# Performance work log

Measured on AMD Instinct MI355X. Metric: run time of the kernel, lower is better.

Reference implementation:

```python
import jax, jax.numpy as jnp
import numpy as np

EPS = 1e-6

def _rmsnorm(h, w):
    # RMSNorm: h * rsqrt(mean(h^2)) * w
    var = jnp.mean(jnp.square(h), axis=-1, keepdims=True)
    return h * jax.lax.rsqrt(var + EPS) * w

def setup_inputs() -> dict:
    key = jax.random.key(0)
    ks = jax.random.split(key, 9)
    B, N, L, D, C = 2, 4096, 256, 2048, 6
    s = 0.02
    return {
        "x": jax.random.normal(ks[0], (B, N, D), jnp.float32),
        "text_emb": jax.random.normal(ks[1], (B, L, D), jnp.float32),
        "Wc": jax.random.normal(ks[2], (C, D), jnp.float32) * s,
        "Wq": jax.random.normal(ks[3], (D, D), jnp.float32) * s,
        "Wk": jax.random.normal(ks[4], (D, D), jnp.float32) * s,
        "Wv": jax.random.normal(ks[5], (D, D), jnp.float32) * s,
        "Wo": jax.random.normal(ks[6], (D, D), jnp.float32) * s,
        "blend_weights": jnp.ones((C,), jnp.float32) / C + jax.random.normal(ks[7], (C,), jnp.float32) * 0.1,
        "surreal_gate": jnp.zeros((1,), jnp.float32),
        "norm_weight": jnp.ones((D,), jnp.float32),
        "is_surreal": 1,
    }

def reference(x, text_emb, Wc, Wq, Wk, Wv, Wo, blend_weights, surreal_gate, norm_weight, is_surreal):
    B, N, D = x.shape
    # soft concept clustering over text tokens
    cluster_logits = jnp.einsum('bld,cd->blc', text_emb, Wc)
    cluster_weights = jax.nn.softmax(cluster_logits, axis=-1)
    concept_reps = jnp.einsum('blc,bld->bcd', cluster_weights, text_emb)  # (B,C,D)
    # SDPA with a single key/value per concept: softmax over 1 key == 1, so the
    # attention output is exactly v broadcast over the N query tokens (q and k
    # cancel out of the math entirely; their grads are zero).
    v = jnp.einsum('bcd,ed->bce', concept_reps, Wv)  # (B,C,D) == per-concept output
    blend = jax.nn.softmax(blend_weights, axis=0)
    fused_bd = jnp.einsum('c,bcd->bd', blend, v)  # (B,D)
    if is_surreal:
        gate = jax.nn.sigmoid(surreal_gate)  # (1,)
        contradiction = jnp.var(v, axis=1, ddof=1)  # torch .var() is unbiased
        fused_bd = fused_bd + gate * contradiction * 0.3
    # broadcast to (B,N,D) as the torch module materializes, then norm + out_proj
    fused = jnp.broadcast_to(fused_bd[:, None, :], (B, N, D))
    out = jnp.einsum('bnd,ed->bne', _rmsnorm(fused, norm_weight), Wo)
    return x + out
```

## Files before the change

kernel.cpp:

```cpp
#include <hip/hip_runtime.h>
#include <hip/hip_bf16.h>

#define BB 2
#define NN 4096
#define LL 256
#define DD 2048
#define CC 6
#define EPSF 1e-6f

__device__ __forceinline__ float dot4(float4 a, float4 b) {
    return a.x * b.x + a.y * b.y + a.z * b.z + a.w * b.w;
}

__device__ __forceinline__ void keep4(float4 v) {
    asm volatile("" :: "v"(v.x), "v"(v.y), "v"(v.z), "v"(v.w));
}

__global__ __launch_bounds__(256) void k_cluster(const float* __restrict__ te,
                                                 const float* __restrict__ Wc,
                                                 float* __restrict__ cw,
                                                 const float4* __restrict__ x4) {
    const int tid = threadIdx.x;
    if (blockIdx.x >= 512) {
        size_t i = (size_t)(blockIdx.x - 512) * 256 + tid;
#pragma unroll
        for (int k = 0; k < 16; ++k, i += 512 * 256) keep4(x4[i]);
        return;
    }
    const int row = blockIdx.x;
    const float4* t4 = (const float4*)(te + (size_t)row * DD);
    float p[CC];
#pragma unroll
    for (int c = 0; c < CC; ++c) p[c] = 0.f;
#pragma unroll
    for (int it = 0; it < 2; ++it) {
        const int i = it * 256 + tid;
        const float4 xv = t4[i];
#pragma unroll
        for (int c = 0; c < CC; ++c)
            p[c] += dot4(xv, ((const float4*)(Wc + (size_t)c * DD))[i]);
    }
#pragma unroll
    for (int c = 0; c < CC; ++c)
        for (int off = 32; off; off >>= 1) p[c] += __shfl_down(p[c], off);
    __shared__ float sred[4][CC];
    const int lane = tid & 63, wid = tid >> 6;
    if (lane == 0) {
#pragma unroll
        for (int c = 0; c < CC; ++c) sred[wid][c] = p[c];
    }
    __syncthreads();
    if (tid == 0) {
        float lg[CC], m = -1e30f;
#pragma unroll
        for (int c = 0; c < CC; ++c) {
            lg[c] = sred[0][c] + sred[1][c] + sred[2][c] + sred[3][c];
            m = fmaxf(m, lg[c]);
        }
        float s = 0.f;
#pragma unroll
        for (int c = 0; c < CC; ++c) { lg[c] = __expf(lg[c] - m); s += lg[c]; }
        const float inv = 1.f / s;
#pragma unroll
        for (int c = 0; c < CC; ++c) cw[row * CC + c] = lg[c] * inv;
    }
}

__global__ __launch_bounds__(256) void k_creps(const float* __restrict__ te,
                                               const float* __restrict__ cw,
                                               float* __restrict__ cr,
                                               const float4* __restrict__ x4) {
    const int tid = threadIdx.x;
    if (blockIdx.x >= 64) {
        const size_t HALF4 = (size_t)BB * NN * DD / 8;
        size_t i = HALF4 + (size_t)(blockIdx.x - 64) * 256 + tid;
#pragma unroll
        for (int k = 0; k < 16; ++k, i += 512 * 256) keep4(x4[i]);
        return;
    }
    const int b = blockIdx.x >> 5;
    const int d0 = (blockIdx.x & 31) * 64;
    const int lane = tid & 63, wid = tid >> 6;
    __shared__ float scw[LL * CC];
    __shared__ float sacc[4][64][CC];
    for (int i = tid; i < LL * CC; i += 256) scw[i] = cw[b * LL * CC + i];
    __syncthreads();
    float acc[CC];
#pragma unroll
    for (int c = 0; c < CC; ++c) acc[c] = 0.f;
    const float* tb = te + ((size_t)b * LL + wid * 64) * DD + d0 + lane;
    for (int l = 0; l < 64; ++l) {
        const float xv = tb[(size_t)l * DD];
        const int gl = wid * 64 + l;
#pragma unroll
        for (int c = 0; c < CC; ++c) acc[c] = fmaf(scw[gl * CC + c], xv, acc[c]);
    }
#pragma unroll
    for (int c = 0; c < CC; ++c) sacc[wid][lane][c] = acc[c];
    __syncthreads();
    if (tid < 64) {
#pragma unroll
        for (int c = 0; c < CC; ++c) {
            const float s = sacc[0][tid][c] + sacc[1][tid][c] +
                            sacc[2][tid][c] + sacc[3][tid][c];
            cr[((size_t)b * CC + c) * DD + d0 + tid] = s;
        }
    }
}

__global__ __launch_bounds__(256) void k_vfuse(const float* __restrict__ cr,
                                               const float* __restrict__ Wv,
                                               const float* __restrict__ blendw,
                                               const float* __restrict__ sgate,
                                               const int* __restrict__ issur,
                                               float* __restrict__ fused,
                                               const float4* __restrict__ Wo4) {
    const int tid = threadIdx.x;
    if (blockIdx.x >= 256) {
        size_t i = (size_t)(blockIdx.x - 256) * 256 + tid;
#pragma unroll
        for (int k = 0; k < 16; ++k, i += 256 * 256) keep4(Wo4[i]);
        return;
    }
    const int lane = tid & 63, wid = tid >> 6;
    const int e0 = blockIdx.x * 8 + wid * 2;
    float acc[BB][2][CC];
#pragma unroll
    for (int b = 0; b < BB; ++b)
#pragma unroll
        for (int j = 0; j < 2; ++j)
#pragma unroll
            for (int c = 0; c < CC; ++c) acc[b][j][c] = 0.f;
#pragma unroll
    for (int it = 0; it < 8; ++it) {
        const int d = it * 256 + lane * 4;
        const float4 w0 = *(const float4*)(Wv + (size_t)e0 * DD + d);
        const float4 w1 = *(const float4*)(Wv + (size_t)(e0 + 1) * DD + d);
#pragma unroll
        for (int b = 0; b < BB; ++b)
#pragma unroll
            for (int c = 0; c < CC; ++c) {
                const float4 cv = *(const float4*)(cr + ((size_t)b * CC + c) * DD + d);
                acc[b][0][c] += dot4(cv, w0);
                acc[b][1][c] += dot4(cv, w1);
            }
    }
#pragma unroll
    for (int b = 0; b < BB; ++b)
#pragma unroll
        for (int j = 0; j < 2; ++j)
#pragma unroll
            for (int c = 0; c < CC; ++c)
                for (int off = 32; off; off >>= 1)
                    acc[b][j][c] += __shfl_down(acc[b][j][c], off);
    if (lane == 0) {
        float bw[CC], m = -1e30f;
#pragma unroll
        for (int c = 0; c < CC; ++c) { bw[c] = blendw[c]; m = fmaxf(m, bw[c]); }
        float s = 0.f;
#pragma unroll
        for (int c = 0; c < CC; ++c) { bw[c] = __expf(bw[c] - m); s += bw[c]; }
        const float inv = 1.f / s;
#pragma unroll
        for (int c = 0; c < CC; ++c) bw[c] *= inv;
        const float gate = 1.f / (1.f + __expf(-sgate[0]));
        const int sur = issur[0];
#pragma unroll
        for (int b = 0; b < BB; ++b)
#pragma unroll
            for (int j = 0; j < 2; ++j) {
                float f = 0.f, mean = 0.f;
#pragma unroll
                for (int c = 0; c < CC; ++c) {
                    f = fmaf(bw[c], acc[b][j][c], f);
                    mean += acc[b][j][c];
                }
                mean *= (1.f / CC);
                float var = 0.f;
#pragma unroll
                for (int c = 0; c < CC; ++c) {
                    const float dv = acc[b][j][c] - mean;
                    var = fmaf(dv, dv, var);
                }
                var *= (1.f / (CC - 1));
                if (sur) f = fmaf(gate * var, 0.3f, f);
                fused[b * DD + e0 + j] = f;
            }
    }
}

__global__ __launch_bounds__(256) void k_rmsout(const float* __restrict__ fused,
                                                const float* __restrict__ nw,
                                                const float* __restrict__ Wo,
                                                float* __restrict__ o) {
    const int tid = threadIdx.x;
    const int lane = tid & 63, wid = tid >> 6;
    float ss[BB];
#pragma unroll
    for (int b = 0; b < BB; ++b) ss[b] = 0.f;
#pragma unroll
    for (int k = 0; k < DD / 256; ++k) {
        const int d = k * 256 + tid;
#pragma unroll
        for (int b = 0; b < BB; ++b) {
            const float v = fused[b * DD + d];
            ss[b] = fmaf(v, v, ss[b]);
        }
    }
#pragma unroll
    for (int b = 0; b < BB; ++b)
        for (int off = 32; off; off >>= 1) ss[b] += __shfl_down(ss[b], off);
    __shared__ float sred[4][BB];
    __shared__ float sscale[BB];
    if (lane == 0) {
#pragma unroll
        for (int b = 0; b < BB; ++b) sred[wid][b] = ss[b];
    }
    __syncthreads();
    if (tid == 0) {
#pragma unroll
        for (int b = 0; b < BB; ++b) {
            const float tot = sred[0][b] + sred[1][b] + sred[2][b] + sred[3][b];
            sscale[b] = rsqrtf(tot * (1.f / DD) + EPSF);
        }
    }
    __syncthreads();
    const int e = blockIdx.x * 4 + wid;
    float acc[BB];
#pragma unroll
    for (int b = 0; b < BB; ++b) acc[b] = 0.f;
#pragma unroll
    for (int it = 0; it < DD / 256; ++it) {
        const int d = it * 256 + lane * 4;
        const float4 wv = *(const float4*)(Wo + (size_t)e * DD + d);
        const float4 nv = *(const float4*)(nw + d);
        float4 t;
        t.x = wv.x * nv.x; t.y = wv.y * nv.y; t.z = wv.z * nv.z; t.w = wv.w * nv.w;
#pragma unroll
        for (int b = 0; b < BB; ++b) {
            const float4 fv = *(const float4*)(fused + (size_t)b * DD + d);
            acc[b] += dot4(fv, t);
        }
    }
#pragma unroll
    for (int b = 0; b < BB; ++b) {
        for (int off = 32; off; off >>= 1) acc[b] += __shfl_down(acc[b], off);
        if (lane == 0) o[b * DD + e] = acc[b] * sscale[b];
    }
}

__global__ __launch_bounds__(256) void k_add(const float* __restrict__ x,
                                             const float* __restrict__ o,
                                             float* __restrict__ out) {
    const float4* x4 = (const float4*)x;
    const float4* o4 = (const float4*)o;
    float4* out4 = (float4*)out;
    size_t f = (size_t)blockIdx.x * 256 + threadIdx.x;
#pragma unroll
    for (int k = 0; k < 8; ++k, f += (size_t)2048 * 256) {
        const int e4 = (int)(f & (DD / 4 - 1));
        const int b = (int)(f >> 21);
        const float4 xv = x4[f];
        const float4 ov = o4[b * (DD / 4) + e4];
        float4 r;
        r.x = xv.x + ov.x; r.y = xv.y + ov.y;
        r.z = xv.z + ov.z; r.w = xv.w + ov.w;
        out4[f] = r;
    }
}

extern "C" void kernel_launch(void* const* d_in, const int* in_sizes, int n_in,
                              void* d_out, int out_size, void* d_ws, size_t ws_size,
                              hipStream_t stream) {
    const float* x  = (const float*)d_in[0];
    const float* te = (const float*)d_in[1];
    const float* Wc = (const float*)d_in[2];
    const float* Wv = (const float*)d_in[5];
    const float* Wo = (const float*)d_in[6];
    const float* bw = (const float*)d_in[7];
    const float* sg = (const float*)d_in[8];
    const float* nw = (const float*)d_in[9];
    const int* isur = (const int*)d_in[10];
    float* out = (float*)d_out;

    float* ws     = (float*)d_ws;
    float* cw     = ws;
    float* cr     = ws + 4096;
    float* fusedv = ws + 4096 + 24576;
    float* o      = fusedv + 4096;

    hipLaunchKernelGGL(k_cluster, dim3(1024), dim3(256), 0, stream,
                       te, Wc, cw, (const float4*)x);
    hipLaunchKernelGGL(k_creps,   dim3(576),  dim3(256), 0, stream,
                       te, cw, cr, (const float4*)x);
    hipLaunchKernelGGL(k_vfuse,   dim3(512),  dim3(256), 0, stream,
                       cr, Wv, bw, sg, isur, fusedv, (const float4*)Wo);
    hipLaunchKernelGGL(k_rmsout,  dim3(DD / 4), dim3(256), 0, stream,
                       fusedv, nw, Wo, o);
    hipLaunchKernelGGL(k_add,     dim3(2048), dim3(256), 0, stream, x, o, out);
}
```

Baseline: 58.06 us.

## Drop cache-prefetch blocks, widen per-wave rows in GEMV kernels, nontemporal add

Removes the extra blocks in the first three kernels that prefetched x and Wo into cache while the small kernels ran. Each wave in the Wv and Wo GEMV kernels now computes four output rows instead of two or one, using fewer blocks and reusing the loaded activation vectors. The final broadcast add uses nontemporal loads and stores. Without the prefetch, x must stream from HBM during the add, and the GEMVs run with lower occupancy across fewer blocks.

```diff
diff --git a/kernel.cpp b/kernel.cpp
--- a/kernel.cpp
+++ b/kernel.cpp
@@ -8,25 +8,16 @@
 #define CC 6
 #define EPSF 1e-6f
 
+typedef float floatx4 __attribute__((ext_vector_type(4)));
+
 __device__ __forceinline__ float dot4(float4 a, float4 b) {
     return a.x * b.x + a.y * b.y + a.z * b.z + a.w * b.w;
 }
 
-__device__ __forceinline__ void keep4(float4 v) {
-    asm volatile("" :: "v"(v.x), "v"(v.y), "v"(v.z), "v"(v.w));
-}
-
 __global__ __launch_bounds__(256) void k_cluster(const float* __restrict__ te,
                                                  const float* __restrict__ Wc,
-                                                 float* __restrict__ cw,
-                                                 const float4* __restrict__ x4) {
-    const int tid = threadIdx.x;
-    if (blockIdx.x >= 512) {
-        size_t i = (size_t)(blockIdx.x - 512) * 256 + tid;
-#pragma unroll
-        for (int k = 0; k < 16; ++k, i += 512 * 256) keep4(x4[i]);
-        return;
-    }
+                                                 float* __restrict__ cw) {
+    const int tid = threadIdx.x;
     const int row = blockIdx.x;
     const float4* t4 = (const float4*)(te + (size_t)row * DD);
     float p[CC];
@@ -68,16 +59,8 @@
 
 __global__ __launch_bounds__(256) void k_creps(const float* __restrict__ te,
                                                const float* __restrict__ cw,
-                                               float* __restrict__ cr,
-                                               const float4* __restrict__ x4) {
-    const int tid = threadIdx.x;
-    if (blockIdx.x >= 64) {
-        const size_t HALF4 = (size_t)BB * NN * DD / 8;
-        size_t i = HALF4 + (size_t)(blockIdx.x - 64) * 256 + tid;
-#pragma unroll
-        for (int k = 0; k < 16; ++k, i += 512 * 256) keep4(x4[i]);
-        return;
-    }
+                                               float* __restrict__ cr) {
+    const int tid = threadIdx.x;
     const int b = blockIdx.x >> 5;
     const int d0 = (blockIdx.x & 31) * 64;
     const int lane = tid & 63, wid = tid >> 6;
@@ -113,42 +96,37 @@
                                                const float* __restrict__ blendw,
                                                const float* __restrict__ sgate,
                                                const int* __restrict__ issur,
-                                               float* __restrict__ fused,
-                                               const float4* __restrict__ Wo4) {
-    const int tid = threadIdx.x;
-    if (blockIdx.x >= 256) {
-        size_t i = (size_t)(blockIdx.x - 256) * 256 + tid;
-#pragma unroll
-        for (int k = 0; k < 16; ++k, i += 256 * 256) keep4(Wo4[i]);
-        return;
-    }
-    const int lane = tid & 63, wid = tid >> 6;
-    const int e0 = blockIdx.x * 8 + wid * 2;
-    float acc[BB][2][CC];
-#pragma unroll
-    for (int b = 0; b < BB; ++b)
-#pragma unroll
-        for (int j = 0; j < 2; ++j)
+                                               float* __restrict__ fused) {
+    const int tid = threadIdx.x;
+    const int lane = tid & 63, wid = tid >> 6;
+    const int e0 = (blockIdx.x * 4 + wid) * 4;
+    float acc[BB][4][CC];
+#pragma unroll
+    for (int b = 0; b < BB; ++b)
+#pragma unroll
+        for (int j = 0; j < 4; ++j)
 #pragma unroll
             for (int c = 0; c < CC; ++c) acc[b][j][c] = 0.f;
 #pragma unroll
     for (int it = 0; it < 8; ++it) {
         const int d = it * 256 + lane * 4;
-        const float4 w0 = *(const float4*)(Wv + (size_t)e0 * DD + d);
-        const float4 w1 = *(const float4*)(Wv + (size_t)(e0 + 1) * DD + d);
+        float4 w[4];
+#pragma unroll
+        for (int j = 0; j < 4; ++j)
+            w[j] = *(const float4*)(Wv + (size_t)(e0 + j) * DD + d);
 #pragma unroll
         for (int b = 0; b < BB; ++b)
 #pragma unroll
             for (int c = 0; c < CC; ++c) {
                 const float4 cv = *(const float4*)(cr + ((size_t)b * CC + c) * DD + d);
-                acc[b][0][c] += dot4(cv, w0);
-                acc[b][1][c] += dot4(cv, w1);
+#pragma unroll
+                for (int j = 0; j < 4; ++j) acc[b][j][c] += dot4(cv, w[j]);
             }
     }
 #pragma unroll
     for (int b = 0; b < BB; ++b)
 #pragma unroll
-        for (int j = 0; j < 2; ++j)
+        for (int j = 0; j < 4; ++j)
 #pragma unroll
             for (int c = 0; c < CC; ++c)
                 for (int off = 32; off; off >>= 1)
@@ -168,7 +146,7 @@
 #pragma unroll
         for (int b = 0; b < BB; ++b)
 #pragma unroll
-            for (int j = 0; j < 2; ++j) {
+            for (int j = 0; j < 4; ++j) {
                 float f = 0.f, mean = 0.f;
 #pragma unroll
                 for (int c = 0; c < CC; ++c) {
@@ -225,47 +203,55 @@
         }
     }
     __syncthreads();
-    const int e = blockIdx.x * 4 + wid;
-    float acc[BB];
-#pragma unroll
-    for (int b = 0; b < BB; ++b) acc[b] = 0.f;
-#pragma unroll
-    for (int it = 0; it < DD / 256; ++it) {
+    const int e0 = (blockIdx.x * 4 + wid) * 4;
+    float acc[BB][4];
+#pragma unroll
+    for (int b = 0; b < BB; ++b)
+#pragma unroll
+        for (int j = 0; j < 4; ++j) acc[b][j] = 0.f;
+#pragma unroll
+    for (int it = 0; it < 8; ++it) {
         const int d = it * 256 + lane * 4;
-        const float4 wv = *(const float4*)(Wo + (size_t)e * DD + d);
         const float4 nv = *(const float4*)(nw + d);
-        float4 t;
-        t.x = wv.x * nv.x; t.y = wv.y * nv.y; t.z = wv.z * nv.z; t.w = wv.w * nv.w;
+        float4 w[4];
+#pragma unroll
+        for (int j = 0; j < 4; ++j) {
+            const float4 wv = *(const float4*)(Wo + (size_t)(e0 + j) * DD + d);
+            w[j].x = wv.x * nv.x; w[j].y = wv.y * nv.y;
+            w[j].z = wv.z * nv.z; w[j].w = wv.w * nv.w;
+        }
 #pragma unroll
         for (int b = 0; b < BB; ++b) {
             const float4 fv = *(const float4*)(fused + (size_t)b * DD + d);
-            acc[b] += dot4(fv, t);
-        }
-    }
-#pragma unroll
-    for (int b = 0; b < BB; ++b) {
-        for (int off = 32; off; off >>= 1) acc[b] += __shfl_down(acc[b], off);
-        if (lane == 0) o[b * DD + e] = acc[b] * sscale[b];
-    }
+#pragma unroll
+            for (int j = 0; j < 4; ++j) acc[b][j] += dot4(fv, w[j]);
+        }
+    }
+#pragma unroll
+    for (int b = 0; b < BB; ++b)
+#pragma unroll
+        for (int j = 0; j < 4; ++j) {
+            float v = acc[b][j];
+            for (int off = 32; off; off >>= 1) v += __shfl_down(v, off);
+            if (lane == 0) o[b * DD + e0 + j] = v * sscale[b];
+        }
 }
 
 __global__ __launch_bounds__(256) void k_add(const float* __restrict__ x,
                                              const float* __restrict__ o,
                                              float* __restrict__ out) {
-    const float4* x4 = (const float4*)x;
-    const float4* o4 = (const float4*)o;
-    float4* out4 = (float4*)out;
+    const floatx4* x4 = (const floatx4*)x;
+    const floatx4* o4 = (const floatx4*)o;
+    floatx4* out4 = (floatx4*)out;
     size_t f = (size_t)blockIdx.x * 256 + threadIdx.x;
 #pragma unroll
     for (int k = 0; k < 8; ++k, f += (size_t)2048 * 256) {
         const int e4 = (int)(f & (DD / 4 - 1));
         const int b = (int)(f >> 21);
-        const float4 xv = x4[f];
-        const float4 ov = o4[b * (DD / 4) + e4];
-        float4 r;
-        r.x = xv.x + ov.x; r.y = xv.y + ov.y;
-        r.z = xv.z + ov.z; r.w = xv.w + ov.w;
-        out4[f] = r;
+        const floatx4 xv = __builtin_nontemporal_load(&x4[f]);
+        const floatx4 ov = o4[b * (DD / 4) + e4];
+        const floatx4 r = xv + ov;
+        __builtin_nontemporal_store(r, &out4[f]);
     }
 }
 
@@ -289,13 +275,11 @@
     float* fusedv = ws + 4096 + 24576;
     float* o      = fusedv + 4096;
 
-    hipLaunchKernelGGL(k_cluster, dim3(1024), dim3(256), 0, stream,
-                       te, Wc, cw, (const float4*)x);
-    hipLaunchKernelGGL(k_creps,   dim3(576),  dim3(256), 0, stream,
-                       te, cw, cr, (const float4*)x);
-    hipLaunchKernelGGL(k_vfuse,   dim3(512),  dim3(256), 0, stream,
-                       cr, Wv, bw, sg, isur, fusedv, (const float4*)Wo);
-    hipLaunchKernelGGL(k_rmsout,  dim3(DD / 4), dim3(256), 0, stream,
+    hipLaunchKernelGGL(k_cluster, dim3(BB * LL), dim3(256), 0, stream, te, Wc, cw);
+    hipLaunchKernelGGL(k_creps,   dim3(BB * 32), dim3(256), 0, stream, te, cw, cr);
+    hipLaunchKernelGGL(k_vfuse,   dim3(128), dim3(256), 0, stream,
+                       cr, Wv, bw, sg, isur, fusedv);
+    hipLaunchKernelGGL(k_rmsout,  dim3(128), dim3(256), 0, stream,
                        fusedv, nw, Wo, o);
     hipLaunchKernelGGL(k_add,     dim3(2048), dim3(256), 0, stream, x, o, out);
 }
```

Measured after the change: 73.68 us. 1.27x slower.

## Fuse front-end stages into one cooperative kernel with grid syncs

Applied to the files above, without the earlier changes.

Replaces the four small pre-processing kernels (cluster softmax, concept reps, V projection/fuse, RMSNorm+out proj) with one cooperative persistent kernel that separates the stages with grid-wide syncs, keeping the old kernels as a fallback. It also drops the L2 prefetch side-blocks (keep4 loads of x and Wo) that were piggybacked on the earlier kernels. The aim is to cut launch gaps between the dependent small stages. In exchange the grid-sync overhead is added, and the lost prefetch of x may make the final add kernel more DRAM-bound.

```diff
diff --git a/kernel.cpp b/kernel.cpp
--- a/kernel.cpp
+++ b/kernel.cpp
@@ -1,5 +1,8 @@
 #include <hip/hip_runtime.h>
 #include <hip/hip_bf16.h>
+#include <hip/hip_cooperative_groups.h>
+
+namespace cg = cooperative_groups;
 
 #define BB 2
 #define NN 4096
@@ -12,21 +15,217 @@
     return a.x * b.x + a.y * b.y + a.z * b.z + a.w * b.w;
 }
 
-__device__ __forceinline__ void keep4(float4 v) {
-    asm volatile("" :: "v"(v.x), "v"(v.y), "v"(v.z), "v"(v.w));
+__global__ __launch_bounds__(256) void k_front(
+    const float* __restrict__ te, const float* __restrict__ Wc,
+    const float* __restrict__ Wv, const float* __restrict__ Wo,
+    const float* __restrict__ blendw, const float* __restrict__ sgate,
+    const int* __restrict__ issur, const float* __restrict__ nw,
+    float* __restrict__ cw, float* __restrict__ cr,
+    float* __restrict__ fused, float* __restrict__ o)
+{
+    cg::grid_group gg = cg::this_grid();
+    __shared__ float smem[3072];
+    const int G = gridDim.x;
+    const int tid = threadIdx.x;
+    const int lane = tid & 63, wid = tid >> 6;
+
+    for (int row = blockIdx.x; row < BB * LL; row += G) {
+        const float4* t4 = (const float4*)(te + (size_t)row * DD);
+        float p[CC];
+#pragma unroll
+        for (int c = 0; c < CC; ++c) p[c] = 0.f;
+#pragma unroll
+        for (int it = 0; it < 2; ++it) {
+            const int i = it * 256 + tid;
+            const float4 xv = t4[i];
+#pragma unroll
+            for (int c = 0; c < CC; ++c)
+                p[c] += dot4(xv, ((const float4*)(Wc + (size_t)c * DD))[i]);
+        }
+#pragma unroll
+        for (int c = 0; c < CC; ++c)
+            for (int off = 32; off; off >>= 1) p[c] += __shfl_down(p[c], off);
+        if (lane == 0) {
+#pragma unroll
+            for (int c = 0; c < CC; ++c) smem[wid * CC + c] = p[c];
+        }
+        __syncthreads();
+        if (tid == 0) {
+            float lg[CC], m = -1e30f;
+#pragma unroll
+            for (int c = 0; c < CC; ++c) {
+                lg[c] = smem[c] + smem[CC + c] + smem[2 * CC + c] + smem[3 * CC + c];
+                m = fmaxf(m, lg[c]);
+            }
+            float s = 0.f;
+#pragma unroll
+            for (int c = 0; c < CC; ++c) { lg[c] = __expf(lg[c] - m); s += lg[c]; }
+            const float inv = 1.f / s;
+#pragma unroll
+            for (int c = 0; c < CC; ++c) cw[row * CC + c] = lg[c] * inv;
+        }
+        __syncthreads();
+    }
+    gg.sync();
+
+    for (int u = blockIdx.x; u < 64; u += G) {
+        const int b = u >> 5;
+        const int d0 = (u & 31) * 64;
+        float* scw = smem;
+        float* sacc = smem + 1536;
+        for (int i = tid; i < LL * CC; i += 256) scw[i] = cw[b * LL * CC + i];
+        __syncthreads();
+        float acc[CC];
+#pragma unroll
+        for (int c = 0; c < CC; ++c) acc[c] = 0.f;
+        const float* tb = te + ((size_t)b * LL + wid * 64) * DD + d0 + lane;
+        for (int l = 0; l < 64; ++l) {
+            const float xv = tb[(size_t)l * DD];
+            const int gl = wid * 64 + l;
+#pragma unroll
+            for (int c = 0; c < CC; ++c) acc[c] = fmaf(scw[gl * CC + c], xv, acc[c]);
+        }
+#pragma unroll
+        for (int c = 0; c < CC; ++c) sacc[(wid * 64 + lane) * CC + c] = acc[c];
+        __syncthreads();
+        if (tid < 64) {
+#pragma unroll
+            for (int c = 0; c < CC; ++c) {
+                const float s = sacc[(0 * 64 + tid) * CC + c] + sacc[(1 * 64 + tid) * CC + c] +
+                                sacc[(2 * 64 + tid) * CC + c] + sacc[(3 * 64 + tid) * CC + c];
+                cr[((size_t)b * CC + c) * DD + d0 + tid] = s;
+            }
+        }
+        __syncthreads();
+    }
+    gg.sync();
+
+    for (int u = blockIdx.x; u < 512; u += G) {
+        const int e = u * 4 + wid;
+        float acc[BB][CC];
+#pragma unroll
+        for (int b = 0; b < BB; ++b)
+#pragma unroll
+            for (int c = 0; c < CC; ++c) acc[b][c] = 0.f;
+#pragma unroll
+        for (int it = 0; it < 8; ++it) {
+            const int d = it * 256 + lane * 4;
+            const float4 wv = *(const float4*)(Wv + (size_t)e * DD + d);
+#pragma unroll
+            for (int b = 0; b < BB; ++b)
+#pragma unroll
+                for (int c = 0; c < CC; ++c) {
+                    const float4 cv = *(const float4*)(cr + ((size_t)b * CC + c) * DD + d);
+                    acc[b][c] += dot4(cv, wv);
+                }
+        }
+#pragma unroll
+        for (int b = 0; b < BB; ++b)
+#pragma unroll
+            for (int c = 0; c < CC; ++c)
+                for (int off = 32; off; off >>= 1)
+                    acc[b][c] += __shfl_down(acc[b][c], off);
+        if (lane == 0) {
+            float bw[CC], m = -1e30f;
+#pragma unroll
+            for (int c = 0; c < CC; ++c) { bw[c] = blendw[c]; m = fmaxf(m, bw[c]); }
+            float s = 0.f;
+#pragma unroll
+            for (int c = 0; c < CC; ++c) { bw[c] = __expf(bw[c] - m); s += bw[c]; }
+            const float inv = 1.f / s;
+#pragma unroll
+            for (int c = 0; c < CC; ++c) bw[c] *= inv;
+            const float gate = 1.f / (1.f + __expf(-sgate[0]));
+            const int sur = issur[0];
+#pragma unroll
+            for (int b = 0; b < BB; ++b) {
+                float f = 0.f, mean = 0.f;
+#pragma unroll
+                for (int c = 0; c < CC; ++c) {
+                    f = fmaf(bw[c], acc[b][c], f);
+                    mean += acc[b][c];
+                }
+                mean *= (1.f / CC);
+                float var = 0.f;
+#pragma unroll
+                for (int c = 0; c < CC; ++c) {
+                    const float dv = acc[b][c] - mean;
+                    var = fmaf(dv, dv, var);
+                }
+                var *= (1.f / (CC - 1));
+                if (sur) f = fmaf(gate * var, 0.3f, f);
+                fused[b * DD + e] = f;
+            }
+        }
+    }
+    gg.sync();
+
+    {
+        float ss[BB];
+#pragma unroll
+        for (int b = 0; b < BB; ++b) ss[b] = 0.f;
+#pragma unroll
+        for (int k = 0; k < DD / 256; ++k) {
+            const int d = k * 256 + tid;
+#pragma unroll
+            for (int b = 0; b < BB; ++b) {
+                const float v = fused[b * DD + d];
+                ss[b] = fmaf(v, v, ss[b]);
+            }
+        }
+#pragma unroll
+        for (int b = 0; b < BB; ++b)
+            for (int off = 32; off; off >>= 1) ss[b] += __shfl_down(ss[b], off);
+        if (lane == 0) {
+#pragma unroll
+            for (int b = 0; b < BB; ++b) smem[wid * BB + b] = ss[b];
+        }
+        __syncthreads();
+        if (tid == 0) {
+#pragma unroll
+            for (int b = 0; b < BB; ++b) {
+                const float tot = smem[0 * BB + b] + smem[1 * BB + b] +
+                                  smem[2 * BB + b] + smem[3 * BB + b];
+                smem[8 + b] = rsqrtf(tot * (1.f / DD) + EPSF);
+            }
+        }
+        __syncthreads();
+        const float scl0 = smem[8], scl1 = smem[9];
+        for (int u = blockIdx.x; u < 512; u += G) {
+            const int e = u * 4 + wid;
+            float acc[BB];
+#pragma unroll
+            for (int b = 0; b < BB; ++b) acc[b] = 0.f;
+#pragma unroll
+            for (int it = 0; it < 8; ++it) {
+                const int d = it * 256 + lane * 4;
+                const float4 wv = *(const float4*)(Wo + (size_t)e * DD + d);
+                const float4 nv = *(const float4*)(nw + d);
+                float4 t;
+                t.x = wv.x * nv.x; t.y = wv.y * nv.y;
+                t.z = wv.z * nv.z; t.w = wv.w * nv.w;
+#pragma unroll
+                for (int b = 0; b < BB; ++b) {
+                    const float4 fv = *(const float4*)(fused + (size_t)b * DD + d);
+                    acc[b] += dot4(fv, t);
+                }
+            }
+#pragma unroll
+            for (int b = 0; b < BB; ++b) {
+                for (int off = 32; off; off >>= 1) acc[b] += __shfl_down(acc[b], off);
+            }
+            if (lane == 0) {
+                o[0 * DD + e] = acc[0] * scl0;
+                o[1 * DD + e] = acc[1] * scl1;
+            }
+        }
+    }
 }
 
 __global__ __launch_bounds__(256) void k_cluster(const float* __restrict__ te,
                                                  const float* __restrict__ Wc,
-                                                 float* __restrict__ cw,
-                                                 const float4* __restrict__ x4) {
+                                                 float* __restrict__ cw) {
     const int tid = threadIdx.x;
-    if (blockIdx.x >= 512) {
-        size_t i = (size_t)(blockIdx.x - 512) * 256 + tid;
-#pragma unroll
-        for (int k = 0; k < 16; ++k, i += 512 * 256) keep4(x4[i]);
-        return;
-    }
     const int row = blockIdx.x;
     const float4* t4 = (const float4*)(te + (size_t)row * DD);
     float p[CC];
@@ -68,16 +267,8 @@
 
 __global__ __launch_bounds__(256) void k_creps(const float* __restrict__ te,
                                                const float* __restrict__ cw,
-                                               float* __restrict__ cr,
-                                               const float4* __restrict__ x4) {
+                                               float* __restrict__ cr) {
     const int tid = threadIdx.x;
-    if (blockIdx.x >= 64) {
-        const size_t HALF4 = (size_t)BB * NN * DD / 8;
-        size_t i = HALF4 + (size_t)(blockIdx.x - 64) * 256 + tid;
-#pragma unroll
-        for (int k = 0; k < 16; ++k, i += 512 * 256) keep4(x4[i]);
-        return;
-    }
     const int b = blockIdx.x >> 5;
     const int d0 = (blockIdx.x & 31) * 64;
     const int lane = tid & 63, wid = tid >> 6;
@@ -113,46 +304,33 @@
                                                const float* __restrict__ blendw,
                                                const float* __restrict__ sgate,
                                                const int* __restrict__ issur,
-                                               float* __restrict__ fused,
-                                               const float4* __restrict__ Wo4) {
+                                               float* __restrict__ fused) {
     const int tid = threadIdx.x;
-    if (blockIdx.x >= 256) {
-        size_t i = (size_t)(blockIdx.x - 256) * 256 + tid;
-#pragma unroll
-        for (int k = 0; k < 16; ++k, i += 256 * 256) keep4(Wo4[i]);
-        return;
-    }
     const int lane = tid & 63, wid = tid >> 6;
-    const int e0 = blockIdx.x * 8 + wid * 2;
-    float acc[BB][2][CC];
+    const int e = blockIdx.x * 4 + wid;
+    float acc[BB][CC];
 #pragma unroll
     for (int b = 0; b < BB; ++b)
 #pragma unroll
-        for (int j = 0; j < 2; ++j)
-#pragma unroll
-            for (int c = 0; c < CC; ++c) acc[b][j][c] = 0.f;
+        for (int c = 0; c < CC; ++c) acc[b][c] = 0.f;
 #pragma unroll
     for (int it = 0; it < 8; ++it) {
         const int d = it * 256 + lane * 4;
-        const float4 w0 = *(const float4*)(Wv + (size_t)e0 * DD + d);
-        const float4 w1 = *(const float4*)(Wv + (size_t)(e0 + 1) * DD + d);
+        const float4 wv = *(const float4*)(Wv + (size_t)e * DD + d);
 #pragma unroll
         for (int b = 0; b < BB; ++b)
 #pragma unroll
             for (int c = 0; c < CC; ++c) {
                 const float4 cv = *(const float4*)(cr + ((size_t)b * CC + c) * DD + d);
-                acc[b][0][c] += dot4(cv, w0);
-                acc[b][1][c] += dot4(cv, w1);
+                acc[b][c] += dot4(cv, wv);
             }
     }
 #pragma unroll
     for (int b = 0; b < BB; ++b)
 #pragma unroll
-        for (int j = 0; j < 2; ++j)
-#pragma unroll
-            for (int c = 0; c < CC; ++c)
-                for (int off = 32; off; off >>= 1)
-                    acc[b][j][c] += __shfl_down(acc[b][j][c], off);
+        for (int c = 0; c < CC; ++c)
+            for (int off = 32; off; off >>= 1)
+                acc[b][c] += __shfl_down(acc[b][c], off);
     if (lane == 0) {
         float bw[CC], m = -1e30f;
 #pragma unroll
@@ -166,26 +344,24 @@
         const float gate = 1.f / (1.f + __expf(-sgate[0]));
         const int sur = issur[0];
 #pragma unroll
-        for (int b = 0; b < BB; ++b)
-#pragma unroll
-            for (int j = 0; j < 2; ++j) {
-                float f = 0.f, mean = 0.f;
-#pragma unroll
-                for (int c = 0; c < CC; ++c) {
-                    f = fmaf(bw[c], acc[b][j][c], f);
-                    mean += acc[b][j][c];
-                }
-                mean *= (1.f / CC);
-                float var = 0.f;
-#pragma unroll
-                for (int c = 0; c < CC; ++c) {
-                    const float dv = acc[b][j][c] - mean;
-                    var = fmaf(dv, dv, var);
-                }
-                var *= (1.f / (CC - 1));
-                if (sur) f = fmaf(gate * var, 0.3f, f);
-                fused[b * DD + e0 + j] = f;
-            }
+        for (int b = 0; b < BB; ++b) {
+            float f = 0.f, mean = 0.f;
+#pragma unroll
+            for (int c = 0; c < CC; ++c) {
+                f = fmaf(bw[c], acc[b][c], f);
+                mean += acc[b][c];
+            }
+            mean *= (1.f / CC);
+            float var = 0.f;
+#pragma unroll
+            for (int c = 0; c < CC; ++c) {
+                const float dv = acc[b][c] - mean;
+                var = fmaf(dv, dv, var);
+            }
+            var *= (1.f / (CC - 1));
+            if (sur) f = fmaf(gate * var, 0.3f, f);
+            fused[b * DD + e] = f;
+        }
     }
 }
 
@@ -230,7 +406,7 @@
 #pragma unroll
     for (int b = 0; b < BB; ++b) acc[b] = 0.f;
 #pragma unroll
-    for (int it = 0; it < DD / 256; ++it) {
+    for (int it = 0; it < 8; ++it) {
         const int d = it * 256 + lane * 4;
         const float4 wv = *(const float4*)(Wo + (size_t)e * DD + d);
         const float4 nv = *(const float4*)(nw + d);
@@ -252,12 +428,12 @@
 __global__ __launch_bounds__(256) void k_add(const float* __restrict__ x,
                                              const float* __restrict__ o,
                                              float* __restrict__ out) {
+    const size_t total4 = (size_t)BB * NN * DD / 4;
     const float4* x4 = (const float4*)x;
     const float4* o4 = (const float4*)o;
     float4* out4 = (float4*)out;
-    size_t f = (size_t)blockIdx.x * 256 + threadIdx.x;
-#pragma unroll
-    for (int k = 0; k < 8; ++k, f += (size_t)2048 * 256) {
+    for (size_t f = (size_t)blockIdx.x * 256 + threadIdx.x; f < total4;
+         f += (size_t)gridDim.x * 256) {
         const int e4 = (int)(f & (DD / 4 - 1));
         const int b = (int)(f >> 21);
         const float4 xv = x4[f];
@@ -289,13 +465,30 @@
     float* fusedv = ws + 4096 + 24576;
     float* o      = fusedv + 4096;
 
-    hipLaunchKernelGGL(k_cluster, dim3(1024), dim3(256), 0, stream,
-                       te, Wc, cw, (const float4*)x);
-    hipLaunchKernelGGL(k_creps,   dim3(576),  dim3(256), 0, stream,
-                       te, cw, cr, (const float4*)x);
-    hipLaunchKernelGGL(k_vfuse,   dim3(512),  dim3(256), 0, stream,
-                       cr, Wv, bw, sg, isur, fusedv, (const float4*)Wo);
-    hipLaunchKernelGGL(k_rmsout,  dim3(DD / 4), dim3(256), 0, stream,
-                       fusedv, nw, Wo, o);
-    hipLaunchKernelGGL(k_add,     dim3(2048), dim3(256), 0, stream, x, o, out);
-}
+    bool launched = false;
+    int nbPerCU = 0;
+    hipError_t qe = hipOccupancyMaxActiveBlocksPerMultiprocessor(
+        &nbPerCU, (const void*)k_front, 256, 0);
+    if (qe == hipSuccess && nbPerCU > 0) {
+        long total = (long)nbPerCU * 256;
+        int grid = (int)(total < 512 ? total : 512);
+        void* args[] = { (void*)&te, (void*)&Wc, (void*)&Wv, (void*)&Wo,
+                         (void*)&bw, (void*)&sg, (void*)&isur, (void*)&nw,
+                         (void*)&cw, (void*)&cr, (void*)&fusedv, (void*)&o };
+        hipError_t le = hipLaunchCooperativeKernel((void*)k_front, dim3(grid),
+                                                   dim3(256), args, 0, stream);
+        if (le == hipSuccess) launched = true;
+        else (void)hipGetLastError();
+    } else {
+        (void)hipGetLastError();
+    }
+    if (!launched) {
+        hipLaunchKernelGGL(k_cluster, dim3(BB * LL), dim3(256), 0, stream, te, Wc, cw);
+        hipLaunchKernelGGL(k_creps,   dim3(BB * 32), dim3(256), 0, stream, te, cw, cr);
+        hipLaunchKernelGGL(k_vfuse,   dim3(DD / 4), dim3(256), 0, stream,
+                           cr, Wv, bw, sg, isur, fusedv);
+        hipLaunchKernelGGL(k_rmsout,  dim3(DD / 4), dim3(256), 0, stream,
+                           fusedv, nw, Wo, o);
+    }
+    hipLaunchKernelGGL(k_add, dim3(2048), dim3(256), 0, stream, x, o, out);
+}
```

Result: faster. 52.18 us (-10.1%).
